# Kernel optimization log

Hardware: AMD Instinct MI355X
Metric: run time of the kernel (lower is better)

The kernel has to match this reference:

```python
import jax, jax.numpy as jnp
import numpy as np

B, T, C = 1, 4096, 1024   # batch, seq, n_embd
E, K = 64, 8              # num_experts, router top-k
G, TG = 8, 4              # n_group, topk_group
H, HS = 512, 2048         # expert hidden, shared-expert hidden
STD = 0.02


def setup_inputs() -> dict:
    key = jax.random.key(0)
    ks = jax.random.split(key, 9)
    return {
        "x": jax.random.normal(ks[0], (B, T, C), jnp.float32),
        "router_w": jax.random.normal(ks[1], (E, C), jnp.float32) * (C ** -0.5),
        "e_bias": jnp.zeros((E,), jnp.float32),  # e_score_correction_bias buffer
        "gate_w": jax.random.normal(ks[2], (E, C, H), jnp.float32) * STD,
        "up_w": jax.random.normal(ks[3], (E, C, H), jnp.float32) * STD,
        "down_w": jax.random.normal(ks[4], (E, H, C), jnp.float32) * STD,
        "sh_gate_w": jax.random.normal(ks[5], (C, HS), jnp.float32) * STD,
        "sh_up_w": jax.random.normal(ks[6], (C, HS), jnp.float32) * STD,
        "sh_down_w": jax.random.normal(ks[7], (HS, C), jnp.float32) * STD,
    }


def _route(xf, router_w, e_bias):
    # grouped sigmoid top-k routing with score-correction bias (group_limited_greedy)
    S = xf.shape[0]
    scores = jax.nn.sigmoid(xf @ router_w.T)          # [S,E], raw sigmoid scores
    sb = scores + e_bias                               # biased scores (selection only)
    epg = E // G
    # per-group score = sum of top (K // topk_group) biased scores in that group
    grp = jax.lax.top_k(sb.reshape(S, G, epg), K // TG)[0].sum(-1)   # [S,G]
    gidx = jax.lax.top_k(grp, TG)[1]                                 # [S,TG]
    gmask = jnp.zeros((S, G), bool).at[jnp.arange(S)[:, None], gidx].set(True)
    emask = jnp.repeat(gmask, epg, axis=1)                           # [S,E]
    masked = jnp.where(emask, sb, -jnp.inf)
    topk_idx = jax.lax.top_k(masked, K)[1]                           # [S,K]
    w = jnp.take_along_axis(scores, topk_idx, axis=1)                # raw scores gathered
    w = w / (w.sum(-1, keepdims=True) + 1e-20)                       # norm_topk_prob
    return topk_idx, w


def reference(x, router_w, e_bias, gate_w, up_w, down_w, sh_gate_w, sh_up_w, sh_down_w):
    Bq, Tq, Cq = x.shape
    xf = x.reshape(Bq * Tq, Cq)
    # always-on shared expert (SwiGLU)
    shared = (jax.nn.silu(xf @ sh_gate_w) * (xf @ sh_up_w)) @ sh_down_w
    topk_idx, w = _route(xf, router_w, e_bias)
    fe = topk_idx.reshape(-1)                          # [S*K] expert id per routed row
    order = jnp.argsort(fe, stable=True)               # sort rows by expert (grouped)
    tok = order // K                                   # source token of each sorted row
    sorted_x = xf[tok]                                 # [S*K, C]
    group_sizes = jnp.bincount(fe, length=E).astype(jnp.int32)
    # grouped GEMMs (== torch._grouped_mm / bmm-over-buckets in the original)
    g = jax.lax.ragged_dot(sorted_x, gate_w, group_sizes)
    u = jax.lax.ragged_dot(sorted_x, up_w, group_sizes)
    h = jax.nn.silu(g) * u
    o = jax.lax.ragged_dot(h, down_w, group_sizes)     # [S*K, C]
    o = o * w.reshape(-1)[order][:, None]              # weight by routing prob
    routed = jnp.zeros_like(xf).at[tok].add(o)         # combine back per token
    return (shared + routed).reshape(Bq, Tq, Cq)
```

## Files before the change

kernel.cpp:

```cpp
#include <hip/hip_runtime.h>
#include <hip/hip_bf16.h>
#include <stdint.h>


#define S_TOK 4096
#define C_DIM 1024
#define E_NUM 64
#define H_DIM 512
#define HS_DIM 2048
#define ROWS_TOTAL (S_TOK * 8)
#define T_TILES 320

typedef __attribute__((ext_vector_type(8))) short short8;
typedef __attribute__((ext_vector_type(4))) float f32x4;

static __device__ __forceinline__ unsigned short f2bf(float f) {
    union { float f; uint32_t u; } v; v.f = f;
    uint32_t u = v.u;
    u += 0x7fffu + ((u >> 16) & 1u);
    return (unsigned short)(u >> 16);
}

static __device__ __forceinline__ void gl2lds16(const void* g, void* l) {
    __builtin_amdgcn_global_load_lds(
        (const __attribute__((address_space(1))) uint32_t*)g,
        (__attribute__((address_space(3))) uint32_t*)l, 16, 0, 0);
}

__global__ __launch_bounds__(256)
void router_scores_k(const float* __restrict__ x, const float* __restrict__ rw,
                     float* __restrict__ scores, int* __restrict__ counts) {
    if (blockIdx.x == 0 && threadIdx.x < E_NUM) counts[threadIdx.x] = 0;
    int t0 = blockIdx.x * 32;
    __shared__ float xs[32][36];
    __shared__ float wsm[64][36];
    int t = threadIdx.x;
    int tx = t & 15, ty = t >> 4;
    float acc[2][4] = {};
    for (int k0 = 0; k0 < C_DIM; k0 += 32) {
        {
            int r = t >> 3, c = t & 7;
            *(float4*)&xs[r][c * 4] = *(const float4*)(x + (size_t)(t0 + r) * C_DIM + k0 + c * 4);
        }
        #pragma unroll
        for (int i = 0; i < 2; i++) {
            int idx = t + 256 * i;
            int r = idx >> 3, c = idx & 7;
            *(float4*)&wsm[r][c * 4] = *(const float4*)(rw + (size_t)r * C_DIM + k0 + c * 4);
        }
        __syncthreads();
        #pragma unroll
        for (int kk = 0; kk < 32; kk += 4) {
            float4 a0 = *(const float4*)&xs[ty * 2 + 0][kk];
            float4 a1 = *(const float4*)&xs[ty * 2 + 1][kk];
            #pragma unroll
            for (int j = 0; j < 4; j++) {
                float4 b = *(const float4*)&wsm[tx * 4 + j][kk];
                acc[0][j] += a0.x * b.x + a0.y * b.y + a0.z * b.z + a0.w * b.w;
                acc[1][j] += a1.x * b.x + a1.y * b.y + a1.z * b.z + a1.w * b.w;
            }
        }
        __syncthreads();
    }
    #pragma unroll
    for (int i = 0; i < 2; i++)
        #pragma unroll
        for (int j = 0; j < 4; j++)
            scores[(size_t)(t0 + ty * 2 + i) * E_NUM + tx * 4 + j] =
                1.f / (1.f + __expf(-acc[i][j]));
}

__global__ __launch_bounds__(256)
void topk_k(const float* __restrict__ scores, const float* __restrict__ ebias,
            int* __restrict__ topk_idx, float* __restrict__ topk_w,
            int* __restrict__ counts) {
    int t = blockIdx.x * 4 + (threadIdx.x >> 6);
    int e = threadIdx.x & 63;
    float sc = scores[(size_t)t * E_NUM + e];
    float sb = sc + ebias[e];
    float m1 = sb, m2 = -1e30f;
    #pragma unroll
    for (int off = 1; off <= 4; off <<= 1) {
        float o1 = __shfl_xor(m1, off);
        float o2 = __shfl_xor(m2, off);
        float hi = fmaxf(m1, o1), lo = fminf(m1, o1);
        m2 = fmaxf(lo, fmaxf(m2, o2));
        m1 = hi;
    }
    float grp = m1 + m2;
    float grpv[8];
    #pragma unroll
    for (int g = 0; g < 8; g++) grpv[g] = __shfl(grp, g * 8);
    unsigned gsel = 0;
    #pragma unroll
    for (int k = 0; k < 4; k++) {
        float best = -1e30f; int bi = 0;
        #pragma unroll
        for (int g = 0; g < 8; g++)
            if (!((gsel >> g) & 1) && grpv[g] > best) { best = grpv[g]; bi = g; }
        gsel |= 1u << bi;
    }
    float val = ((gsel >> (e >> 3)) & 1) ? sb : -1e30f;
    int idx[8]; float sv[8]; float wsum = 0.f;
    #pragma unroll
    for (int k = 0; k < 8; k++) {
        uint32_t u = __float_as_uint(val);
        uint32_t mu = (u & 0x80000000u) ? ~u : (u | 0x80000000u);
        unsigned long long key = ((unsigned long long)mu << 6) | (unsigned long long)(63 - e);
        #pragma unroll
        for (int off = 32; off; off >>= 1) {
            unsigned long long ok = __shfl_xor(key, off);
            if (ok > key) key = ok;
        }
        int win = 63 - (int)(key & 63ull);
        idx[k] = win;
        sv[k] = __shfl(sc, win);
        wsum += sv[k];
        if (e == win) val = -1e30f;
    }
    float inv = 1.f / (wsum + 1e-20f);
    if (e < 8) {
        topk_idx[t * 8 + e] = idx[e];
        topk_w[t * 8 + e] = sv[e] * inv;
        atomicAdd(&counts[idx[e]], 1);
    }
}

__global__ void scan_k(const int* __restrict__ counts, int* __restrict__ base,
                       int* __restrict__ cursor, int* __restrict__ tile_e,
                       int* __restrict__ tile_m0) {
    int e = threadIdx.x;
    int c = counts[e];
    int s = c;
    #pragma unroll
    for (int off = 1; off < 64; off <<= 1) {
        int o = __shfl_up(s, off);
        if (e >= off) s += o;
    }
    int ex = s - c;
    base[e] = ex;
    cursor[e] = ex;
    int nt = (c + 127) >> 7;
    int ts = nt;
    #pragma unroll
    for (int off = 1; off < 64; off <<= 1) {
        int o = __shfl_up(ts, off);
        if (e >= off) ts += o;
    }
    int tb = ts - nt;
    for (int i = 0; i < nt; i++) { tile_e[tb + i] = e; tile_m0[tb + i] = i * 128; }
    int total = __shfl(ts, 63);
    for (int j = total + e; j < T_TILES; j += 64) tile_e[j] = -1;
}

__global__ void scatter_k(const int* __restrict__ topk_idx, const float* __restrict__ topk_w,
                          int* __restrict__ cursor, int* __restrict__ row_token,
                          float* __restrict__ row_wgt, int* __restrict__ pos_of) {
    int i = blockIdx.x * blockDim.x + threadIdx.x;
    int e = topk_idx[i];
    int pos = atomicAdd(&cursor[e], 1);
    row_token[pos] = i >> 3;
    row_wgt[pos] = topk_w[i];
    pos_of[i] = pos;
}

__global__ __launch_bounds__(256)
void combine_k(const float* __restrict__ O, const int* __restrict__ pos_of,
               float* __restrict__ out) {
    int t = blockIdx.x;
    int c = threadIdx.x;
    float4 s = ((const float4*)(out + (size_t)t * C_DIM))[c];
    int p[8];
    #pragma unroll
    for (int k = 0; k < 8; k++) p[k] = pos_of[t * 8 + k];
    #pragma unroll
    for (int k = 0; k < 8; k++) {
        float4 v = ((const float4*)(O + (size_t)p[k] * C_DIM))[c];
        s.x += v.x; s.y += v.y; s.z += v.z; s.w += v.w;
    }
    ((float4*)(out + (size_t)t * C_DIM))[c] = s;
}

__global__ void cvt_bf16_k(const float* __restrict__ in, unsigned short* __restrict__ out, int n8) {
    int i = blockIdx.x * blockDim.x + threadIdx.x;
    if (i >= n8) return;
    float4 v0 = ((const float4*)in)[2 * i];
    float4 v1 = ((const float4*)in)[2 * i + 1];
    unsigned short t[8] = { f2bf(v0.x), f2bf(v0.y), f2bf(v0.z), f2bf(v0.w),
                            f2bf(v1.x), f2bf(v1.y), f2bf(v1.z), f2bf(v1.w) };
    ((uint4*)out)[i] = *(uint4*)t;
}

#define TP 69
__global__ __launch_bounds__(256)
void transpose_k(const float* __restrict__ in, unsigned short* __restrict__ out, int R, int C) {
    size_t bofs = (size_t)blockIdx.z * R * C;
    in += bofs; out += bofs;
    int r0 = blockIdx.y * 64, c0 = blockIdx.x * 64;
    __shared__ float T[64 * TP];
    int t = threadIdx.x;
    int cg = t & 15, rg = t >> 4;
    #pragma unroll
    for (int ii = 0; ii < 4; ii++) {
        float4 v = *(const float4*)(in + (size_t)(r0 + rg * 4 + ii) * C + c0 + cg * 4);
        T[(cg * 4 + 0) * TP + rg * 4 + ii] = v.x;
        T[(cg * 4 + 1) * TP + rg * 4 + ii] = v.y;
        T[(cg * 4 + 2) * TP + rg * 4 + ii] = v.z;
        T[(cg * 4 + 3) * TP + rg * 4 + ii] = v.w;
    }
    __syncthreads();
    int n = t >> 2, ks = (t & 3) * 16;
    unsigned short h[16];
    #pragma unroll
    for (int u = 0; u < 16; u++) h[u] = f2bf(T[n * TP + ks + u]);
    unsigned short* op = out + (size_t)(c0 + n) * R + r0 + ks;
    *(uint4*)op = *(uint4*)&h[0];
    *(uint4*)(op + 8) = *(uint4*)&h[8];
}

template<bool FUSED, bool GATHER, bool WL, int EPI>
__global__ __launch_bounds__(256, 3)
void gemm2_k(const short* __restrict__ A, const short* __restrict__ B1t,
             const short* __restrict__ B2t, void* __restrict__ Cout,
             int M, int N, int K,
             const int* __restrict__ counts, const int* __restrict__ base,
             const int* __restrict__ row_token, const float* __restrict__ row_wgt,
             const int* __restrict__ tile_e, const int* __restrict__ tile_m0) {
    constexpr int BN = FUSED ? 64 : 128;
    constexpr int NJ = FUSED ? 2 : 4;

    int e = 0, m0, Mrows, rowbase = 0;
    if (WL) {
        e = tile_e[blockIdx.y];
        if (e < 0) return;
        m0 = tile_m0[blockIdx.y];
        Mrows = counts[e];
        rowbase = base[e];
    } else {
        m0 = blockIdx.y * 128;
        Mrows = M;
    }
    int n0 = blockIdx.x * BN;
    const short* B1 = B1t + (WL ? (size_t)e * N * K : 0) + (size_t)n0 * K;
    const short* B2 = FUSED ? (B2t + (WL ? (size_t)e * N * K : 0) + (size_t)n0 * K) : nullptr;

    __shared__ short As[3 * 4096];
    __shared__ short Bs1[FUSED ? 3 * 2048 : 3 * 4096];
    __shared__ short Bs2[FUSED ? 3 * 2048 : 16];

    int tid = threadIdx.x;
    int lane = tid & 63, w = tid >> 6;
    int wr = w >> 1, wc = w & 1;
    int quad = lane >> 4, l16 = lane & 15;
    int sr = lane >> 2, sc = lane & 3;

    const short* aptr[2];
    const short* b1ptr[2];
    const short* b2ptr;
    #pragma unroll
    for (int i = 0; i < 2; i++) {
        int row = w * 32 + i * 16 + sr;
        int mrow = m0 + row;
        int cl = mrow < Mrows ? mrow : (Mrows - 1);
        size_t arow;
        if (GATHER)  arow = (size_t)row_token[rowbase + cl];
        else if (WL) arow = (size_t)(rowbase + cl);
        else         arow = (size_t)mrow;
        aptr[i] = A + arow * K + sc * 8;
    }
    if constexpr (FUSED) {
        int row = w * 16 + sr;
        b1ptr[0] = B1 + (size_t)row * K + sc * 8;
        b2ptr    = B2 + (size_t)row * K + sc * 8;
    } else {
        #pragma unroll
        for (int i = 0; i < 2; i++) {
            int row = w * 32 + i * 16 + sr;
            b1ptr[i] = B1 + (size_t)row * K + sc * 8;
        }
        b2ptr = nullptr;
    }

    f32x4 acc1[4][NJ] = {};
    f32x4 acc2[FUSED ? 4 : 1][NJ] = {};

    const int nk = K >> 5;
    auto stage = [&](int slot) {
        #pragma unroll
        for (int i = 0; i < 2; i++) {
            gl2lds16(aptr[i], &As[slot * 4096 + (w * 32 + i * 16) * 32]);
            aptr[i] += 32;
        }
        if constexpr (FUSED) {
            gl2lds16(b1ptr[0], &Bs1[slot * 2048 + w * 512]); b1ptr[0] += 32;
            gl2lds16(b2ptr,    &Bs2[slot * 2048 + w * 512]); b2ptr += 32;
        } else {
            #pragma unroll
            for (int i = 0; i < 2; i++) {
                gl2lds16(b1ptr[i], &Bs1[slot * 4096 + (w * 32 + i * 16) * 32]);
                b1ptr[i] += 32;
            }
        }
    };
    stage(0);
    if (nk > 1) stage(1);

    int slot = 0, nslot = 2;
    for (int t = 0; t < nk; t++) {
        if (t + 1 < nk) {
            asm volatile("s_waitcnt vmcnt(4)" ::: "memory");
        } else {
            asm volatile("s_waitcnt vmcnt(0)" ::: "memory");
        }
        __builtin_amdgcn_s_barrier();
        __builtin_amdgcn_sched_barrier(0);

        if (t + 2 < nk) stage(nslot);

        short8 a[4], b1[NJ], b2[NJ];
        #pragma unroll
        for (int i = 0; i < 4; i++)
            a[i] = *(const short8*)&As[slot * 4096 + (wr * 64 + i * 16 + l16) * 32 + quad * 8];
        if constexpr (FUSED) {
            #pragma unroll
            for (int j = 0; j < NJ; j++) {
                b1[j] = *(const short8*)&Bs1[slot * 2048 + (wc * 32 + j * 16 + l16) * 32 + quad * 8];
                b2[j] = *(const short8*)&Bs2[slot * 2048 + (wc * 32 + j * 16 + l16) * 32 + quad * 8];
            }
        } else {
            #pragma unroll
            for (int j = 0; j < NJ; j++)
                b1[j] = *(const short8*)&Bs1[slot * 4096 + (wc * 64 + j * 16 + l16) * 32 + quad * 8];
        }
        #pragma unroll
        for (int i = 0; i < 4; i++)
            #pragma unroll
            for (int j = 0; j < NJ; j++) {
                acc1[i][j] = __builtin_amdgcn_mfma_f32_16x16x32_bf16(a[i], b1[j], acc1[i][j], 0, 0, 0);
                if (FUSED)
                    acc2[i][j] = __builtin_amdgcn_mfma_f32_16x16x32_bf16(a[i], b2[j], acc2[i][j], 0, 0, 0);
            }
        slot = (slot == 2) ? 0 : slot + 1;
        nslot = (nslot == 2) ? 0 : nslot + 1;
    }

    constexpr int CB = FUSED ? 32 : 64;
    #pragma unroll
    for (int i = 0; i < 4; i++) {
        #pragma unroll
        for (int rr = 0; rr < 4; rr++) {
            int row = m0 + wr * 64 + i * 16 + quad * 4 + rr;
            if (row >= Mrows) continue;
            size_t orow = WL ? (size_t)(rowbase + row) : (size_t)row;
            float scl = 0.f;
            if (EPI == 2) scl = row_wgt[rowbase + row];
            #pragma unroll
            for (int j = 0; j < NJ; j++) {
                int n = n0 + wc * CB + j * 16 + l16;
                float v = acc1[i][j][rr];
                if (EPI == 0) {
                    float u = acc2[i][j][rr];
                    float h = v / (1.f + __expf(-v)) * u;
                    ((unsigned short*)Cout)[orow * N + n] = f2bf(h);
                } else if (EPI == 1) {
                    ((float*)Cout)[orow * N + n] = v;
                } else {
                    ((float*)Cout)[orow * N + n] = v * scl;
                }
            }
        }
    }
}

extern "C" void kernel_launch(void* const* d_in, const int* in_sizes, int n_in,
                              void* d_out, int out_size, void* d_ws, size_t ws_size,
                              hipStream_t stream) {
    const float* x        = (const float*)d_in[0];
    const float* router_w = (const float*)d_in[1];
    const float* e_bias   = (const float*)d_in[2];
    const float* gate_w   = (const float*)d_in[3];
    const float* up_w     = (const float*)d_in[4];
    const float* down_w   = (const float*)d_in[5];
    const float* sh_gate  = (const float*)d_in[6];
    const float* sh_up    = (const float*)d_in[7];
    const float* sh_down  = (const float*)d_in[8];
    float* out = (float*)d_out;
    char* ws = (char*)d_ws;

    int*   counts    = (int*)(ws);
    int*   base      = (int*)(ws + 256);
    int*   cursor    = (int*)(ws + 512);
    int*   topk_idx  = (int*)(ws + 1024);
    float* topk_w    = (float*)(ws + 1024 + 131072);
    int*   row_token = (int*)(ws + 1024 + 2 * 131072);
    float* row_wgt   = (float*)(ws + 1024 + 3 * 131072);
    float* scoresbuf = (float*)(ws + 1024 + 4 * 131072);
    int*   pos_of    = (int*)(ws + 1664 * 1024);
    int*   tile_e    = (int*)(ws + 1800 * 1024);
    int*   tile_m0   = (int*)(ws + 1808 * 1024);
    const size_t MB = 1u << 20;
    unsigned short* xb        = (unsigned short*)(ws + 2 * MB);
    unsigned short* Hs        = (unsigned short*)(ws + 10 * MB);
    unsigned short* Hr        = (unsigned short*)(ws + 26 * MB);
    unsigned short* sh_gate_t = (unsigned short*)(ws + 58 * MB);
    unsigned short* sh_up_t   = (unsigned short*)(ws + 62 * MB);
    unsigned short* sh_down_t = (unsigned short*)(ws + 66 * MB);
    unsigned short* gate_t    = (unsigned short*)(ws + 70 * MB);
    unsigned short* up_t      = (unsigned short*)(ws + 134 * MB);
    unsigned short* down_t    = (unsigned short*)(ws + 198 * MB);
    float* O = (float*)(ws + 70 * MB);

    router_scores_k<<<S_TOK / 32, 256, 0, stream>>>(x, router_w, scoresbuf, counts);
    topk_k<<<S_TOK / 4, 256, 0, stream>>>(scoresbuf, e_bias, topk_idx, topk_w, counts);
    scan_k<<<1, 64, 0, stream>>>(counts, base, cursor, tile_e, tile_m0);
    scatter_k<<<ROWS_TOTAL / 256, 256, 0, stream>>>(topk_idx, topk_w, cursor, row_token, row_wgt, pos_of);

    cvt_bf16_k<<<S_TOK * C_DIM / 8 / 256, 256, 0, stream>>>(x, xb, S_TOK * C_DIM / 8);
    transpose_k<<<dim3(HS_DIM / 64, C_DIM / 64, 1), 256, 0, stream>>>(sh_gate, sh_gate_t, C_DIM, HS_DIM);
    transpose_k<<<dim3(HS_DIM / 64, C_DIM / 64, 1), 256, 0, stream>>>(sh_up,   sh_up_t,   C_DIM, HS_DIM);
    transpose_k<<<dim3(C_DIM / 64, HS_DIM / 64, 1), 256, 0, stream>>>(sh_down, sh_down_t, HS_DIM, C_DIM);
    transpose_k<<<dim3(H_DIM / 64, C_DIM / 64, E_NUM), 256, 0, stream>>>(gate_w, gate_t, C_DIM, H_DIM);
    transpose_k<<<dim3(H_DIM / 64, C_DIM / 64, E_NUM), 256, 0, stream>>>(up_w,   up_t,   C_DIM, H_DIM);
    transpose_k<<<dim3(C_DIM / 64, H_DIM / 64, E_NUM), 256, 0, stream>>>(down_w, down_t, H_DIM, C_DIM);

    gemm2_k<true, false, false, 0><<<dim3(HS_DIM / 64, S_TOK / 128, 1), 256, 0, stream>>>(
        (const short*)xb, (const short*)sh_gate_t, (const short*)sh_up_t, Hs,
        S_TOK, HS_DIM, C_DIM, nullptr, nullptr, nullptr, nullptr, nullptr, nullptr);
    gemm2_k<false, false, false, 1><<<dim3(C_DIM / 128, S_TOK / 128, 1), 256, 0, stream>>>(
        (const short*)Hs, (const short*)sh_down_t, nullptr, out,
        S_TOK, C_DIM, HS_DIM, nullptr, nullptr, nullptr, nullptr, nullptr, nullptr);

    gemm2_k<true, true, true, 0><<<dim3(H_DIM / 64, T_TILES, 1), 256, 0, stream>>>(
        (const short*)xb, (const short*)gate_t, (const short*)up_t, Hr,
        0, H_DIM, C_DIM, counts, base, row_token, row_wgt, tile_e, tile_m0);
    gemm2_k<false, false, true, 2><<<dim3(C_DIM / 128, T_TILES, 1), 256, 0, stream>>>(
        (const short*)Hr, (const short*)down_t, nullptr, O,
        0, C_DIM, H_DIM, counts, base, row_token, row_wgt, tile_e, tile_m0);

    combine_k<<<S_TOK, 256, 0, stream>>>(O, pos_of, out);
}
```

Baseline: 940.9 us.

## Fuse fp32 weight transpose and bf16 conversion into GEMM B-tile loading

Drops the six transpose_k pre-passes, which wrote bf16 transposed copies of all expert and shared weights. The GEMM now reads fp32 weights in their original [K,N] layout through registers, converts them to bf16 and writes them into XOR-swizzled LDS. The pipeline changes from a 3-slot async global-to-LDS ring to double buffering with register prefetch and __syncthreads. The aim is to remove the extra weight read/write passes, at the cost of reading fp32 weights (twice the bytes) inside every GEMM tile, repeated for each M tile, and a shallower pipeline.

Result: faster. 881.4 us (-6.3%).

```diff
diff --git a/kernel.cpp b/kernel.cpp
--- a/kernel.cpp
+++ b/kernel.cpp
@@ -191,43 +191,17 @@
     ((uint4*)out)[i] = *(uint4*)t;
 }
 
-#define TP 69
-__global__ __launch_bounds__(256)
-void transpose_k(const float* __restrict__ in, unsigned short* __restrict__ out, int R, int C) {
-    size_t bofs = (size_t)blockIdx.z * R * C;
-    in += bofs; out += bofs;
-    int r0 = blockIdx.y * 64, c0 = blockIdx.x * 64;
-    __shared__ float T[64 * TP];
-    int t = threadIdx.x;
-    int cg = t & 15, rg = t >> 4;
-    #pragma unroll
-    for (int ii = 0; ii < 4; ii++) {
-        float4 v = *(const float4*)(in + (size_t)(r0 + rg * 4 + ii) * C + c0 + cg * 4);
-        T[(cg * 4 + 0) * TP + rg * 4 + ii] = v.x;
-        T[(cg * 4 + 1) * TP + rg * 4 + ii] = v.y;
-        T[(cg * 4 + 2) * TP + rg * 4 + ii] = v.z;
-        T[(cg * 4 + 3) * TP + rg * 4 + ii] = v.w;
-    }
-    __syncthreads();
-    int n = t >> 2, ks = (t & 3) * 16;
-    unsigned short h[16];
-    #pragma unroll
-    for (int u = 0; u < 16; u++) h[u] = f2bf(T[n * TP + ks + u]);
-    unsigned short* op = out + (size_t)(c0 + n) * R + r0 + ks;
-    *(uint4*)op = *(uint4*)&h[0];
-    *(uint4*)(op + 8) = *(uint4*)&h[8];
-}
-
 template<bool FUSED, bool GATHER, bool WL, int EPI>
 __global__ __launch_bounds__(256, 3)
-void gemm2_k(const short* __restrict__ A, const short* __restrict__ B1t,
-             const short* __restrict__ B2t, void* __restrict__ Cout,
+void gemm2_k(const short* __restrict__ A, const float* __restrict__ B1f,
+             const float* __restrict__ B2f, void* __restrict__ Cout,
              int M, int N, int K,
              const int* __restrict__ counts, const int* __restrict__ base,
              const int* __restrict__ row_token, const float* __restrict__ row_wgt,
              const int* __restrict__ tile_e, const int* __restrict__ tile_m0) {
     constexpr int BN = FUSED ? 64 : 128;
     constexpr int NJ = FUSED ? 2 : 4;
+    constexpr int BS = BN * 32;
 
     int e = 0, m0, Mrows, rowbase = 0;
     if (WL) {
@@ -241,12 +215,12 @@
         Mrows = M;
     }
     int n0 = blockIdx.x * BN;
-    const short* B1 = B1t + (WL ? (size_t)e * N * K : 0) + (size_t)n0 * K;
-    const short* B2 = FUSED ? (B2t + (WL ? (size_t)e * N * K : 0) + (size_t)n0 * K) : nullptr;
-
-    __shared__ short As[3 * 4096];
-    __shared__ short Bs1[FUSED ? 3 * 2048 : 3 * 4096];
-    __shared__ short Bs2[FUSED ? 3 * 2048 : 16];
+    const float* B1 = B1f + (WL ? (size_t)e * N * K : 0);
+    const float* B2 = FUSED ? (B2f + (WL ? (size_t)e * N * K : 0)) : nullptr;
+
+    __shared__ short As[2 * 4096];
+    __shared__ short Bs1[2 * BS];
+    __shared__ short Bs2[FUSED ? 2 * BS : 16];
 
     int tid = threadIdx.x;
     int lane = tid & 63, w = tid >> 6;
@@ -255,8 +229,6 @@
     int sr = lane >> 2, sc = lane & 3;
 
     const short* aptr[2];
-    const short* b1ptr[2];
-    const short* b2ptr;
     #pragma unroll
     for (int i = 0; i < 2; i++) {
         int row = w * 32 + i * 16 + sr;
@@ -268,69 +240,73 @@
         else         arow = (size_t)mrow;
         aptr[i] = A + arow * K + sc * 8;
     }
-    if constexpr (FUSED) {
-        int row = w * 16 + sr;
-        b1ptr[0] = B1 + (size_t)row * K + sc * 8;
-        b2ptr    = B2 + (size_t)row * K + sc * 8;
-    } else {
-        #pragma unroll
-        for (int i = 0; i < 2; i++) {
-            int row = w * 32 + i * 16 + sr;
-            b1ptr[i] = B1 + (size_t)row * K + sc * 8;
-        }
-        b2ptr = nullptr;
-    }
+
+    int nb = tid & 63, kg = tid >> 6;
+    const float* b1g = B1 + (size_t)(kg * 8) * N + n0 + nb;
+    const float* b2g = FUSED ? (B2 + (size_t)(kg * 8) * N + n0 + nb) : nullptr;
+    const int bwr = nb * 32 + ((kg * 8) ^ ((nb & 3) << 3));
 
     f32x4 acc1[4][NJ] = {};
     f32x4 acc2[FUSED ? 4 : 1][NJ] = {};
 
     const int nk = K >> 5;
-    auto stage = [&](int slot) {
+
+    auto stageA = [&](int buf) {
         #pragma unroll
         for (int i = 0; i < 2; i++) {
-            gl2lds16(aptr[i], &As[slot * 4096 + (w * 32 + i * 16) * 32]);
+            gl2lds16(aptr[i], &As[buf * 4096 + (w * 32 + i * 16) * 32]);
             aptr[i] += 32;
         }
+    };
+    auto loadB = [&](float (&fb)[2][8]) {
+        #pragma unroll
+        for (int jj = 0; jj < 8; jj++) fb[0][jj] = b1g[(size_t)jj * N];
         if constexpr (FUSED) {
-            gl2lds16(b1ptr[0], &Bs1[slot * 2048 + w * 512]); b1ptr[0] += 32;
-            gl2lds16(b2ptr,    &Bs2[slot * 2048 + w * 512]); b2ptr += 32;
+            #pragma unroll
+            for (int jj = 0; jj < 8; jj++) fb[1][jj] = b2g[(size_t)jj * N];
+            b2g += (size_t)32 * N;
         } else {
             #pragma unroll
-            for (int i = 0; i < 2; i++) {
-                gl2lds16(b1ptr[i], &Bs1[slot * 4096 + (w * 32 + i * 16) * 32]);
-                b1ptr[i] += 32;
-            }
-        }
+            for (int jj = 0; jj < 8; jj++) fb[1][jj] = b1g[(size_t)jj * N + 64];
+        }
+        b1g += (size_t)32 * N;
     };
-    stage(0);
-    if (nk > 1) stage(1);
-
-    int slot = 0, nslot = 2;
+    auto writeB = [&](int buf, float (&fb)[2][8]) {
+        short8 v0, v1;
+        #pragma unroll
+        for (int jj = 0; jj < 8; jj++) {
+            v0[jj] = (short)f2bf(fb[0][jj]);
+            v1[jj] = (short)f2bf(fb[1][jj]);
+        }
+        *(short8*)&Bs1[buf * BS + bwr] = v0;
+        if constexpr (FUSED) *(short8*)&Bs2[buf * BS + bwr] = v1;
+        else                 *(short8*)&Bs1[buf * BS + bwr + 64 * 32] = v1;
+    };
+
+    stageA(0);
+    {
+        float fb[2][8];
+        loadB(fb);
+        writeB(0, fb);
+    }
+    __syncthreads();
+
     for (int t = 0; t < nk; t++) {
-        if (t + 1 < nk) {
-            asm volatile("s_waitcnt vmcnt(4)" ::: "memory");
-        } else {
-            asm volatile("s_waitcnt vmcnt(0)" ::: "memory");
-        }
-        __builtin_amdgcn_s_barrier();
-        __builtin_amdgcn_sched_barrier(0);
-
-        if (t + 2 < nk) stage(nslot);
+        int buf = t & 1;
+        bool more = (t + 1 < nk);
+        float fb[2][8];
+        if (more) { stageA(buf ^ 1); loadB(fb); }
 
         short8 a[4], b1[NJ], b2[NJ];
         #pragma unroll
         for (int i = 0; i < 4; i++)
-            a[i] = *(const short8*)&As[slot * 4096 + (wr * 64 + i * 16 + l16) * 32 + quad * 8];
-        if constexpr (FUSED) {
-            #pragma unroll
-            for (int j = 0; j < NJ; j++) {
-                b1[j] = *(const short8*)&Bs1[slot * 2048 + (wc * 32 + j * 16 + l16) * 32 + quad * 8];
-                b2[j] = *(const short8*)&Bs2[slot * 2048 + (wc * 32 + j * 16 + l16) * 32 + quad * 8];
-            }
-        } else {
-            #pragma unroll
-            for (int j = 0; j < NJ; j++)
-                b1[j] = *(const short8*)&Bs1[slot * 4096 + (wc * 64 + j * 16 + l16) * 32 + quad * 8];
+            a[i] = *(const short8*)&As[buf * 4096 + (wr * 64 + i * 16 + l16) * 32 + quad * 8];
+        #pragma unroll
+        for (int j = 0; j < NJ; j++) {
+            int row = wc * (BN / 2) + j * 16 + l16;
+            int ro = row * 32 + ((quad * 8) ^ ((row & 3) << 3));
+            b1[j] = *(const short8*)&Bs1[buf * BS + ro];
+            if constexpr (FUSED) b2[j] = *(const short8*)&Bs2[buf * BS + ro];
         }
         #pragma unroll
         for (int i = 0; i < 4; i++)
@@ -340,11 +316,11 @@
                 if (FUSED)
                     acc2[i][j] = __builtin_amdgcn_mfma_f32_16x16x32_bf16(a[i], b2[j], acc2[i][j], 0, 0, 0);
             }
-        slot = (slot == 2) ? 0 : slot + 1;
-        nslot = (nslot == 2) ? 0 : nslot + 1;
-    }
-
-    constexpr int CB = FUSED ? 32 : 64;
+        if (more) writeB(buf ^ 1, fb);
+        __syncthreads();
+    }
+
+    constexpr int CB = BN / 2;
     #pragma unroll
     for (int i = 0; i < 4; i++) {
         #pragma unroll
@@ -399,16 +375,10 @@
     int*   tile_e    = (int*)(ws + 1800 * 1024);
     int*   tile_m0   = (int*)(ws + 1808 * 1024);
     const size_t MB = 1u << 20;
-    unsigned short* xb        = (unsigned short*)(ws + 2 * MB);
-    unsigned short* Hs        = (unsigned short*)(ws + 10 * MB);
-    unsigned short* Hr        = (unsigned short*)(ws + 26 * MB);
-    unsigned short* sh_gate_t = (unsigned short*)(ws + 58 * MB);
-    unsigned short* sh_up_t   = (unsigned short*)(ws + 62 * MB);
-    unsigned short* sh_down_t = (unsigned short*)(ws + 66 * MB);
-    unsigned short* gate_t    = (unsigned short*)(ws + 70 * MB);
-    unsigned short* up_t      = (unsigned short*)(ws + 134 * MB);
-    unsigned short* down_t    = (unsigned short*)(ws + 198 * MB);
-    float* O = (float*)(ws + 70 * MB);
+    unsigned short* xb = (unsigned short*)(ws + 2 * MB);
+    unsigned short* Hs = (unsigned short*)(ws + 10 * MB);
+    unsigned short* Hr = (unsigned short*)(ws + 26 * MB);
+    float*          O  = (float*)(ws + 70 * MB);
 
     router_scores_k<<<S_TOK / 32, 256, 0, stream>>>(x, router_w, scoresbuf, counts);
     topk_k<<<S_TOK / 4, 256, 0, stream>>>(scoresbuf, e_bias, topk_idx, topk_w, counts);
@@ -416,25 +386,19 @@
     scatter_k<<<ROWS_TOTAL / 256, 256, 0, stream>>>(topk_idx, topk_w, cursor, row_token, row_wgt, pos_of);
 
     cvt_bf16_k<<<S_TOK * C_DIM / 8 / 256, 256, 0, stream>>>(x, xb, S_TOK * C_DIM / 8);
-    transpose_k<<<dim3(HS_DIM / 64, C_DIM / 64, 1), 256, 0, stream>>>(sh_gate, sh_gate_t, C_DIM, HS_DIM);
-    transpose_k<<<dim3(HS_DIM / 64, C_DIM / 64, 1), 256, 0, stream>>>(sh_up,   sh_up_t,   C_DIM, HS_DIM);
-    transpose_k<<<dim3(C_DIM / 64, HS_DIM / 64, 1), 256, 0, stream>>>(sh_down, sh_down_t, HS_DIM, C_DIM);
-    transpose_k<<<dim3(H_DIM / 64, C_DIM / 64, E_NUM), 256, 0, stream>>>(gate_w, gate_t, C_DIM, H_DIM);
-    transpose_k<<<dim3(H_DIM / 64, C_DIM / 64, E_NUM), 256, 0, stream>>>(up_w,   up_t,   C_DIM, H_DIM);
-    transpose_k<<<dim3(C_DIM / 64, H_DIM / 64, E_NUM), 256, 0, stream>>>(down_w, down_t, H_DIM, C_DIM);
 
     gemm2_k<true, false, false, 0><<<dim3(HS_DIM / 64, S_TOK / 128, 1), 256, 0, stream>>>(
-        (const short*)xb, (const short*)sh_gate_t, (const short*)sh_up_t, Hs,
+        (const short*)xb, sh_gate, sh_up, Hs,
         S_TOK, HS_DIM, C_DIM, nullptr, nullptr, nullptr, nullptr, nullptr, nullptr);
     gemm2_k<false, false, false, 1><<<dim3(C_DIM / 128, S_TOK / 128, 1), 256, 0, stream>>>(
-        (const short*)Hs, (const short*)sh_down_t, nullptr, out,
+        (const short*)Hs, sh_down, nullptr, out,
         S_TOK, C_DIM, HS_DIM, nullptr, nullptr, nullptr, nullptr, nullptr, nullptr);
 
     gemm2_k<true, true, true, 0><<<dim3(H_DIM / 64, T_TILES, 1), 256, 0, stream>>>(
-        (const short*)xb, (const short*)gate_t, (const short*)up_t, Hr,
+        (const short*)xb, gate_w, up_w, Hr,
         0, H_DIM, C_DIM, counts, base, row_token, row_wgt, tile_e, tile_m0);
     gemm2_k<false, false, true, 2><<<dim3(C_DIM / 128, T_TILES, 1), 256, 0, stream>>>(
-        (const short*)Hr, (const short*)down_t, nullptr, O,
+        (const short*)Hr, down_w, nullptr, O,
         0, C_DIM, H_DIM, counts, base, row_token, row_wgt, tile_e, tile_m0);
 
     combine_k<<<S_TOK, 256, 0, stream>>>(O, pos_of, out);
```

## Drop weight transposes; read K-major B tiles via ds_read_b64_tr_b16

Applied to the files above, without the earlier changes.

Replaces the per-call fp32-to-bf16 transpose kernels for all expert and shared weights with plain elementwise bf16 conversion, keeping weights in their original [K,N] layout. The GEMM B-tile loader is rewritten to stage row-major K×N chunks into LDS, and the MFMA B operands are fetched with the transposing LDS read instruction. This removes the LDS-heavy transpose pass over roughly 200MB of weights in exchange for a new LDS layout and an explicit lgkmcnt wait before the MFMAs, which may reduce overlap inside the GEMM loop.

Measured after the change: 943.5 us. About the same (+0.3%).

```diff
diff --git a/kernel.cpp b/kernel.cpp
--- a/kernel.cpp
+++ b/kernel.cpp
@@ -13,6 +13,7 @@
 
 typedef __attribute__((ext_vector_type(8))) short short8;
 typedef __attribute__((ext_vector_type(4))) float f32x4;
+typedef __attribute__((ext_vector_type(2))) unsigned int uint2v;
 
 static __device__ __forceinline__ unsigned short f2bf(float f) {
     union { float f; uint32_t u; } v; v.f = f;
@@ -25,6 +26,12 @@
     __builtin_amdgcn_global_load_lds(
         (const __attribute__((address_space(1))) uint32_t*)g,
         (__attribute__((address_space(3))) uint32_t*)l, 16, 0, 0);
+}
+
+static __device__ __forceinline__ uint2v tr64(unsigned addr) {
+    uint2v r;
+    asm volatile("ds_read_b64_tr_b16 %0, %1" : "=v"(r) : "v"(addr));
+    return r;
 }
 
 __global__ __launch_bounds__(256)
@@ -191,43 +198,18 @@
     ((uint4*)out)[i] = *(uint4*)t;
 }
 
-#define TP 69
-__global__ __launch_bounds__(256)
-void transpose_k(const float* __restrict__ in, unsigned short* __restrict__ out, int R, int C) {
-    size_t bofs = (size_t)blockIdx.z * R * C;
-    in += bofs; out += bofs;
-    int r0 = blockIdx.y * 64, c0 = blockIdx.x * 64;
-    __shared__ float T[64 * TP];
-    int t = threadIdx.x;
-    int cg = t & 15, rg = t >> 4;
-    #pragma unroll
-    for (int ii = 0; ii < 4; ii++) {
-        float4 v = *(const float4*)(in + (size_t)(r0 + rg * 4 + ii) * C + c0 + cg * 4);
-        T[(cg * 4 + 0) * TP + rg * 4 + ii] = v.x;
-        T[(cg * 4 + 1) * TP + rg * 4 + ii] = v.y;
-        T[(cg * 4 + 2) * TP + rg * 4 + ii] = v.z;
-        T[(cg * 4 + 3) * TP + rg * 4 + ii] = v.w;
-    }
-    __syncthreads();
-    int n = t >> 2, ks = (t & 3) * 16;
-    unsigned short h[16];
-    #pragma unroll
-    for (int u = 0; u < 16; u++) h[u] = f2bf(T[n * TP + ks + u]);
-    unsigned short* op = out + (size_t)(c0 + n) * R + r0 + ks;
-    *(uint4*)op = *(uint4*)&h[0];
-    *(uint4*)(op + 8) = *(uint4*)&h[8];
-}
-
 template<bool FUSED, bool GATHER, bool WL, int EPI>
 __global__ __launch_bounds__(256, 3)
-void gemm2_k(const short* __restrict__ A, const short* __restrict__ B1t,
-             const short* __restrict__ B2t, void* __restrict__ Cout,
+void gemm2_k(const short* __restrict__ A, const short* __restrict__ B1b,
+             const short* __restrict__ B2b, void* __restrict__ Cout,
              int M, int N, int K,
              const int* __restrict__ counts, const int* __restrict__ base,
              const int* __restrict__ row_token, const float* __restrict__ row_wgt,
              const int* __restrict__ tile_e, const int* __restrict__ tile_m0) {
     constexpr int BN = FUSED ? 64 : 128;
     constexpr int NJ = FUSED ? 2 : 4;
+    constexpr int NC = BN / 16;
+    constexpr int BS = BN * 32;
 
     int e = 0, m0, Mrows, rowbase = 0;
     if (WL) {
@@ -241,8 +223,8 @@
         Mrows = M;
     }
     int n0 = blockIdx.x * BN;
-    const short* B1 = B1t + (WL ? (size_t)e * N * K : 0) + (size_t)n0 * K;
-    const short* B2 = FUSED ? (B2t + (WL ? (size_t)e * N * K : 0) + (size_t)n0 * K) : nullptr;
+    const short* B1 = B1b + (WL ? (size_t)e * N * K : 0);
+    const short* B2 = FUSED ? (B2b + (WL ? (size_t)e * N * K : 0)) : nullptr;
 
     __shared__ short As[3 * 4096];
     __shared__ short Bs1[FUSED ? 3 * 2048 : 3 * 4096];
@@ -255,8 +237,6 @@
     int sr = lane >> 2, sc = lane & 3;
 
     const short* aptr[2];
-    const short* b1ptr[2];
-    const short* b2ptr;
     #pragma unroll
     for (int i = 0; i < 2; i++) {
         int row = w * 32 + i * 16 + sr;
@@ -268,17 +248,26 @@
         else         arow = (size_t)mrow;
         aptr[i] = A + arow * K + sc * 8;
     }
-    if constexpr (FUSED) {
-        int row = w * 16 + sr;
-        b1ptr[0] = B1 + (size_t)row * K + sc * 8;
-        b2ptr    = B2 + (size_t)row * K + sc * 8;
-    } else {
-        #pragma unroll
-        for (int i = 0; i < 2; i++) {
-            int row = w * 32 + i * 16 + sr;
-            b1ptr[i] = B1 + (size_t)row * K + sc * 8;
-        }
-        b2ptr = nullptr;
+
+    const short* b1ptr[2];
+    const short* b2ptr;
+    {
+        int L = lane;
+        int r = (L & 7) >> 1, c = (L & 1) * 8;
+        if constexpr (FUSED) {
+            int kc = w * 2 + (L >> 5);
+            int nc = (L >> 3) & 3;
+            b1ptr[0] = B1 + (size_t)(kc * 4 + r) * N + n0 + nc * 16 + c;
+            b2ptr    = B2 + (size_t)(kc * 4 + r) * N + n0 + nc * 16 + c;
+        } else {
+            int nc = L >> 3;
+            #pragma unroll
+            for (int i = 0; i < 2; i++) {
+                int kc = w * 2 + i;
+                b1ptr[i] = B1 + (size_t)(kc * 4 + r) * N + n0 + nc * 16 + c;
+            }
+            b2ptr = nullptr;
+        }
     }
 
     f32x4 acc1[4][NJ] = {};
@@ -292,18 +281,29 @@
             aptr[i] += 32;
         }
         if constexpr (FUSED) {
-            gl2lds16(b1ptr[0], &Bs1[slot * 2048 + w * 512]); b1ptr[0] += 32;
-            gl2lds16(b2ptr,    &Bs2[slot * 2048 + w * 512]); b2ptr += 32;
+            gl2lds16(b1ptr[0], &Bs1[slot * 2048 + w * 512]); b1ptr[0] += 32 * N;
+            gl2lds16(b2ptr,    &Bs2[slot * 2048 + w * 512]); b2ptr += 32 * N;
         } else {
             #pragma unroll
             for (int i = 0; i < 2; i++) {
-                gl2lds16(b1ptr[i], &Bs1[slot * 4096 + (w * 32 + i * 16) * 32]);
-                b1ptr[i] += 32;
+                gl2lds16(b1ptr[i], &Bs1[slot * 4096 + (w * 2 + i) * 512]);
+                b1ptr[i] += 32 * N;
             }
         }
     };
     stage(0);
     if (nk > 1) stage(1);
+
+    unsigned trb1 = (unsigned)(size_t)&Bs1[0] + (unsigned)(quad * 2 * NC * 128 + l16 * 8);
+    unsigned trb2 = FUSED ? ((unsigned)(size_t)&Bs2[0] + (unsigned)(quad * 2 * NC * 128 + l16 * 8)) : 0u;
+    auto rdB = [&](unsigned trb, int slot, int nb) -> short8 {
+        unsigned a0 = trb + (unsigned)(slot * BS * 2 + nb * 128);
+        uint2v lo = tr64(a0);
+        uint2v hi = tr64(a0 + NC * 128);
+        union { uint32_t u[4]; short8 s; } u;
+        u.u[0] = lo[0]; u.u[1] = lo[1]; u.u[2] = hi[0]; u.u[3] = hi[1];
+        return u.s;
+    };
 
     int slot = 0, nslot = 2;
     for (int t = 0; t < nk; t++) {
@@ -321,17 +321,14 @@
         #pragma unroll
         for (int i = 0; i < 4; i++)
             a[i] = *(const short8*)&As[slot * 4096 + (wr * 64 + i * 16 + l16) * 32 + quad * 8];
-        if constexpr (FUSED) {
-            #pragma unroll
-            for (int j = 0; j < NJ; j++) {
-                b1[j] = *(const short8*)&Bs1[slot * 2048 + (wc * 32 + j * 16 + l16) * 32 + quad * 8];
-                b2[j] = *(const short8*)&Bs2[slot * 2048 + (wc * 32 + j * 16 + l16) * 32 + quad * 8];
-            }
-        } else {
-            #pragma unroll
-            for (int j = 0; j < NJ; j++)
-                b1[j] = *(const short8*)&Bs1[slot * 4096 + (wc * 64 + j * 16 + l16) * 32 + quad * 8];
-        }
+        #pragma unroll
+        for (int j = 0; j < NJ; j++) {
+            int nb = wc * (BN / 32) + j;
+            b1[j] = rdB(trb1, slot, nb);
+            if constexpr (FUSED) b2[j] = rdB(trb2, slot, nb);
+        }
+        asm volatile("s_waitcnt lgkmcnt(0)" ::: "memory");
+        __builtin_amdgcn_sched_barrier(0);
         #pragma unroll
         for (int i = 0; i < 4; i++)
             #pragma unroll
@@ -344,7 +341,7 @@
         nslot = (nslot == 2) ? 0 : nslot + 1;
     }
 
-    constexpr int CB = FUSED ? 32 : 64;
+    constexpr int CB = BN / 2;
     #pragma unroll
     for (int i = 0; i < 4; i++) {
         #pragma unroll
@@ -402,12 +399,12 @@
     unsigned short* xb        = (unsigned short*)(ws + 2 * MB);
     unsigned short* Hs        = (unsigned short*)(ws + 10 * MB);
     unsigned short* Hr        = (unsigned short*)(ws + 26 * MB);
-    unsigned short* sh_gate_t = (unsigned short*)(ws + 58 * MB);
-    unsigned short* sh_up_t   = (unsigned short*)(ws + 62 * MB);
-    unsigned short* sh_down_t = (unsigned short*)(ws + 66 * MB);
-    unsigned short* gate_t    = (unsigned short*)(ws + 70 * MB);
-    unsigned short* up_t      = (unsigned short*)(ws + 134 * MB);
-    unsigned short* down_t    = (unsigned short*)(ws + 198 * MB);
+    unsigned short* sh_gate_b = (unsigned short*)(ws + 58 * MB);
+    unsigned short* sh_up_b   = (unsigned short*)(ws + 62 * MB);
+    unsigned short* sh_down_b = (unsigned short*)(ws + 66 * MB);
+    unsigned short* gate_b    = (unsigned short*)(ws + 70 * MB);
+    unsigned short* up_b      = (unsigned short*)(ws + 134 * MB);
+    unsigned short* down_b    = (unsigned short*)(ws + 198 * MB);
     float* O = (float*)(ws + 70 * MB);
 
     router_scores_k<<<S_TOK / 32, 256, 0, stream>>>(x, router_w, scoresbuf, counts);
@@ -416,25 +413,27 @@
     scatter_k<<<ROWS_TOTAL / 256, 256, 0, stream>>>(topk_idx, topk_w, cursor, row_token, row_wgt, pos_of);
 
     cvt_bf16_k<<<S_TOK * C_DIM / 8 / 256, 256, 0, stream>>>(x, xb, S_TOK * C_DIM / 8);
-    transpose_k<<<dim3(HS_DIM / 64, C_DIM / 64, 1), 256, 0, stream>>>(sh_gate, sh_gate_t, C_DIM, HS_DIM);
-    transpose_k<<<dim3(HS_DIM / 64, C_DIM / 64, 1), 256, 0, stream>>>(sh_up,   sh_up_t,   C_DIM, HS_DIM);
-    transpose_k<<<dim3(C_DIM / 64, HS_DIM / 64, 1), 256, 0, stream>>>(sh_down, sh_down_t, HS_DIM, C_DIM);
-    transpose_k<<<dim3(H_DIM / 64, C_DIM / 64, E_NUM), 256, 0, stream>>>(gate_w, gate_t, C_DIM, H_DIM);
-    transpose_k<<<dim3(H_DIM / 64, C_DIM / 64, E_NUM), 256, 0, stream>>>(up_w,   up_t,   C_DIM, H_DIM);
-    transpose_k<<<dim3(C_DIM / 64, H_DIM / 64, E_NUM), 256, 0, stream>>>(down_w, down_t, H_DIM, C_DIM);
+    const int NW = E_NUM * C_DIM * H_DIM / 8;
+    cvt_bf16_k<<<NW / 256, 256, 0, stream>>>(gate_w, gate_b, NW);
+    cvt_bf16_k<<<NW / 256, 256, 0, stream>>>(up_w,   up_b,   NW);
+    cvt_bf16_k<<<NW / 256, 256, 0, stream>>>(down_w, down_b, NW);
+    const int NS = C_DIM * HS_DIM / 8;
+    cvt_bf16_k<<<NS / 256, 256, 0, stream>>>(sh_gate, sh_gate_b, NS);
+    cvt_bf16_k<<<NS / 256, 256, 0, stream>>>(sh_up,   sh_up_b,   NS);
+    cvt_bf16_k<<<NS / 256, 256, 0, stream>>>(sh_down, sh_down_b, NS);
 
     gemm2_k<true, false, false, 0><<<dim3(HS_DIM / 64, S_TOK / 128, 1), 256, 0, stream>>>(
-        (const short*)xb, (const short*)sh_gate_t, (const short*)sh_up_t, Hs,
+        (const short*)xb, (const short*)sh_gate_b, (const short*)sh_up_b, Hs,
         S_TOK, HS_DIM, C_DIM, nullptr, nullptr, nullptr, nullptr, nullptr, nullptr);
     gemm2_k<false, false, false, 1><<<dim3(C_DIM / 128, S_TOK / 128, 1), 256, 0, stream>>>(
-        (const short*)Hs, (const short*)sh_down_t, nullptr, out,
+        (const short*)Hs, (const short*)sh_down_b, nullptr, out,
         S_TOK, C_DIM, HS_DIM, nullptr, nullptr, nullptr, nullptr, nullptr, nullptr);
 
     gemm2_k<true, true, true, 0><<<dim3(H_DIM / 64, T_TILES, 1), 256, 0, stream>>>(
-        (const short*)xb, (const short*)gate_t, (const short*)up_t, Hr,
+        (const short*)xb, (const short*)gate_b, (const short*)up_b, Hr,
         0, H_DIM, C_DIM, counts, base, row_token, row_wgt, tile_e, tile_m0);
     gemm2_k<false, false, true, 2><<<dim3(C_DIM / 128, T_TILES, 1), 256, 0, stream>>>(
-        (const short*)Hr, (const short*)down_t, nullptr, O,
+        (const short*)Hr, (const short*)down_b, nullptr, O,
         0, C_DIM, H_DIM, counts, base, row_token, row_wgt, tile_e, tile_m0);
 
     combine_k<<<S_TOK, 256, 0, stream>>>(O, pos_of, out);
```
